# Kernel tuning notes

Measured on AMD Instinct MI355X. Metric: run time of the kernel, lower is better.

## Reference

```python
import jax, jax.numpy as jnp
import numpy as np

B, T, D, H, L, V = 2, 1024, 1024, 4, 4, 32000  # H redefined below
H = 16            # n_heads
HD = D // H       # head_size = 64
NL = 4            # n_layer
EPS = 1e-5


def _layernorm(x, scale, bias):
    mu = jnp.mean(x, axis=-1, keepdims=True)
    var = jnp.mean(jnp.square(x - mu), axis=-1, keepdims=True)
    return (x - mu) * jax.lax.rsqrt(var + EPS) * scale + bias


def setup_inputs() -> dict:
    key = jax.random.key(0)
    ks = iter(jax.random.split(key, 40))
    s = lambda shape: jax.random.normal(next(ks), shape, jnp.float32) * 0.02
    inp = {
        'idx': jax.random.randint(next(ks), (B, T), 0, V),
        'tok_emb': s((V, D)),
        'pos_emb': s((T, D)),
        # per-layer stacked params (leading axis = layer)
        'Wq': s((NL, D, D)), 'Wk': s((NL, D, D)), 'Wv': s((NL, D, D)),
        'Wo': s((NL, D, D)), 'bo': jnp.zeros((NL, D), jnp.float32),
        'ln1_s': jnp.ones((NL, D), jnp.float32), 'ln1_b': jnp.zeros((NL, D), jnp.float32),
        'ln2_s': jnp.ones((NL, D), jnp.float32), 'ln2_b': jnp.zeros((NL, D), jnp.float32),
        'W1': s((NL, D, 4 * D)), 'b1': jnp.zeros((NL, 4 * D), jnp.float32),
        'W2': s((NL, 4 * D, D)), 'b2': jnp.zeros((NL, D), jnp.float32),
        'lnf_s': jnp.ones((D,), jnp.float32), 'lnf_b': jnp.zeros((D,), jnp.float32),
        'Wlm': s((D, V)), 'blm': jnp.zeros((V,), jnp.float32),
    }
    return inp


def reference(idx, tok_emb, pos_emb, Wq, Wk, Wv, Wo, bo,
              ln1_s, ln1_b, ln2_s, ln2_b, W1, b1, W2, b2,
              lnf_s, lnf_b, Wlm, blm):
    b, t = idx.shape
    x = tok_emb[idx] + pos_emb[None, :t]            # [B,T,D]
    causal = jnp.tril(jnp.ones((t, t), bool))        # [T,T]
    scale = 1.0 / np.sqrt(HD).astype(np.float32)
    for l in range(NL):
        h = _layernorm(x, ln1_s[l], ln1_b[l])
        q = (h @ Wq[l]).reshape(b, t, H, HD)
        k = (h @ Wk[l]).reshape(b, t, H, HD)
        v = (h @ Wv[l]).reshape(b, t, H, HD)
        scores = jnp.einsum('bthd,bshd->bhts', q, k) * scale
        scores = jnp.where(causal[None, None], scores, -jnp.inf)
        attn = jax.nn.softmax(scores, axis=-1)       # [B,H,T,T]
        o = jnp.einsum('bhts,bshd->bthd', attn, v).reshape(b, t, D)
        x = x + o @ Wo[l] + bo[l]
        h2 = _layernorm(x, ln2_s[l], ln2_b[l])
        x = x + jax.nn.relu(h2 @ W1[l] + b1[l]) @ W2[l] + b2[l]
    x = _layernorm(x, lnf_s, lnf_b)
    logits = x @ Wlm + blm                           # [B,T,V]
    return logits
```

## Files before the change

### kernel.cpp

```cpp
#include <hip/hip_runtime.h>

typedef unsigned short u16;
typedef unsigned int u32;
typedef __bf16 bf16x8 __attribute__((ext_vector_type(8)));
typedef float f32x4 __attribute__((ext_vector_type(4)));
typedef u16 u16x8 __attribute__((ext_vector_type(8)));
typedef u16 u16x4 __attribute__((ext_vector_type(4)));

static __device__ __forceinline__ u16 f2bf(float f) {
  u32 u = __builtin_bit_cast(u32, f);
  u32 r = (u + 0x7FFFu + ((u >> 16) & 1u)) >> 16;
  return (u16)r;
}

static __device__ __forceinline__ void atomAddF32(float* p, float v) {
  asm volatile("global_atomic_add_f32 %0, %1, off" :: "v"(p), "v"(v) : "memory");
}

#define GLOAD_LDS16(gp, lp)                                                   \
  __builtin_amdgcn_global_load_lds(                                           \
      (const __attribute__((address_space(1))) void*)(gp),                    \
      (__attribute__((address_space(3))) void*)(lp), 16, 0, 0)

#define MFB(a, b, cc) __builtin_amdgcn_mfma_f32_16x16x32_bf16(a, b, cc, 0, 0, 0)

__global__ void k_embed_ln(const int* __restrict__ idx, const float* __restrict__ tok,
                           const float* __restrict__ pos, const float* __restrict__ sc,
                           const float* __restrict__ bi, float* __restrict__ x,
                           u16* __restrict__ out) {
  int row = blockIdx.x;
  int tt = row & 1023;
  int id = idx[row];
  int t = threadIdx.x;
  float4 a = *(const float4*)(tok + (size_t)id * 1024 + t * 4);
  float4 p = *(const float4*)(pos + (size_t)tt * 1024 + t * 4);
  float4 v{a.x + p.x, a.y + p.y, a.z + p.z, a.w + p.w};
  *(float4*)(x + (size_t)row * 1024 + t * 4) = v;
  float s = v.x + v.y + v.z + v.w;
  float ss = v.x * v.x + v.y * v.y + v.z * v.z + v.w * v.w;
  for (int d = 1; d < 64; d <<= 1) { s += __shfl_xor(s, d); ss += __shfl_xor(ss, d); }
  __shared__ float red[8];
  int wave = t >> 6, lane = t & 63;
  if (lane == 0) { red[wave] = s; red[wave + 4] = ss; }
  __syncthreads();
  s = red[0] + red[1] + red[2] + red[3];
  ss = red[4] + red[5] + red[6] + red[7];
  float mu = s * (1.0f / 1024.0f);
  float var = ss * (1.0f / 1024.0f) - mu * mu;
  float inv = rsqrtf(var + 1e-5f);
  float4 g = *(const float4*)(sc + t * 4);
  float4 b = *(const float4*)(bi + t * 4);
  u16x4 o;
  o[0] = f2bf((v.x - mu) * inv * g.x + b.x);
  o[1] = f2bf((v.y - mu) * inv * g.y + b.y);
  o[2] = f2bf((v.z - mu) * inv * g.z + b.z);
  o[3] = f2bf((v.w - mu) * inv * g.w + b.w);
  *(u16x4*)(out + (size_t)row * 1024 + t * 4) = o;
}

__global__ void k_ln(const float* __restrict__ x, const float* __restrict__ sc,
                     const float* __restrict__ bi, u16* __restrict__ out) {
  int row = blockIdx.x;
  int t = threadIdx.x;
  const float* xr = x + (size_t)row * 1024;
  float4 v = *(const float4*)(xr + t * 4);
  float s = v.x + v.y + v.z + v.w;
  float ss = v.x * v.x + v.y * v.y + v.z * v.z + v.w * v.w;
  for (int d = 1; d < 64; d <<= 1) { s += __shfl_xor(s, d); ss += __shfl_xor(ss, d); }
  __shared__ float red[8];
  int wave = t >> 6, lane = t & 63;
  if (lane == 0) { red[wave] = s; red[wave + 4] = ss; }
  __syncthreads();
  s = red[0] + red[1] + red[2] + red[3];
  ss = red[4] + red[5] + red[6] + red[7];
  float mu = s * (1.0f / 1024.0f);
  float var = ss * (1.0f / 1024.0f) - mu * mu;
  float inv = rsqrtf(var + 1e-5f);
  float4 g = *(const float4*)(sc + t * 4);
  float4 b = *(const float4*)(bi + t * 4);
  u16x4 o;
  o[0] = f2bf((v.x - mu) * inv * g.x + b.x);
  o[1] = f2bf((v.y - mu) * inv * g.y + b.y);
  o[2] = f2bf((v.z - mu) * inv * g.z + b.z);
  o[3] = f2bf((v.w - mu) * inv * g.w + b.w);
  *(u16x4*)(out + (size_t)row * 1024 + t * 4) = o;
}

__launch_bounds__(1024)
__global__ void k_transpose(const float* __restrict__ src, u16* __restrict__ dst,
                            int R, int C) {
  __shared__ float tile[32][33];
  int tx = threadIdx.x, ty = threadIdx.y;
  int c = blockIdx.x * 32 + tx;
  int r = blockIdx.y * 32 + ty;
  tile[ty][tx] = src[(size_t)r * C + c];
  __syncthreads();
  int dr = blockIdx.x * 32 + ty;
  int dc = blockIdx.y * 32 + tx;
  dst[(size_t)dr * R + dc] = f2bf(tile[tx][ty]);
}

__launch_bounds__(1024)
__global__ void k_transpose_layer(const float* __restrict__ Wq, const float* __restrict__ Wk,
                                  const float* __restrict__ Wv, const float* __restrict__ Wo,
                                  const float* __restrict__ W1, const float* __restrict__ W2,
                                  u16* __restrict__ qkvT, u16* __restrict__ WoT,
                                  u16* __restrict__ W1T, u16* __restrict__ W2T) {
  int bid = blockIdx.x;
  const float* src; u16* dst; int R, C, bx, by;
  if (bid < 4096) {
    int which = bid >> 10, tile_i = bid & 1023;
    bx = tile_i & 31; by = tile_i >> 5; R = 1024; C = 1024;
    src = which == 0 ? Wq : which == 1 ? Wk : which == 2 ? Wv : Wo;
    dst = which == 3 ? WoT : qkvT + (size_t)which * 1048576;
  } else if (bid < 8192) {
    int tile_i = bid - 4096; bx = tile_i & 127; by = tile_i >> 7; R = 1024; C = 4096;
    src = W1; dst = W1T;
  } else {
    int tile_i = bid - 8192; bx = tile_i & 31; by = tile_i >> 5; R = 4096; C = 1024;
    src = W2; dst = W2T;
  }
  __shared__ float tile[32][33];
  int tx = threadIdx.x, ty = threadIdx.y;
  int c = bx * 32 + tx, r = by * 32 + ty;
  tile[ty][tx] = src[(size_t)r * C + c];
  __syncthreads();
  int dr = bx * 32 + ty, dc = by * 32 + tx;
  dst[(size_t)dr * R + dc] = f2bf(tile[tx][ty]);
}

enum { EPI_QKV = 0, EPI_RELU = 2 };

template <int EPI>
__launch_bounds__(256, 4)
__global__ void k_gemm64(const u16* __restrict__ A, const u16* __restrict__ Bt,
                         const float* __restrict__ bias, u16* __restrict__ bout,
                         int M, int N, int K) {
  __shared__ alignas(16) u16 smem[12288];
#define AL(s, r, k) smem[(s)*2048 + (r)*32 + (k)]
#define BL(s, r, k) smem[4096 + (s)*4096 + (r)*32 + (k)]
  const int t = threadIdx.x;
  const int wave = t >> 6, lane = t & 63;
  const int wm = wave >> 1, wn = wave & 1;
  const int g = lane >> 4, c = lane & 15;
  const int m0 = blockIdx.x * 64, n0 = blockIdx.y * 128;

  const int rwA = t >> 2, sgA = (t & 3) * 8;
  const u16* gA = A + (size_t)(m0 + rwA) * K + sgA;
  const u16* gB = Bt + (size_t)(n0 + rwA) * K + sgA;

  f32x4 acc[2][4] = {};
  const int nK = K >> 5;
  int cur = 0;

  GLOAD_LDS16(gA, &AL(0, rwA, 0));
#pragma unroll
  for (int p = 0; p < 2; ++p)
    GLOAD_LDS16(gB + (size_t)p * 64 * K, &BL(0, p * 64 + rwA, 0));
  __syncthreads();

  for (int kt = 0; kt < nK; ++kt) {
    if (kt + 1 < nK) {
      const int k0 = (kt + 1) << 5;
      GLOAD_LDS16(gA + k0, &AL(cur ^ 1, rwA, 0));
#pragma unroll
      for (int p = 0; p < 2; ++p)
        GLOAD_LDS16(gB + k0 + (size_t)p * 64 * K, &BL(cur ^ 1, p * 64 + rwA, 0));
    }
    bf16x8 af[2], bfr[4];
#pragma unroll
    for (int i = 0; i < 2; ++i)
      af[i] = *(const bf16x8*)&AL(cur, wm * 32 + i * 16 + c, g * 8);
#pragma unroll
    for (int j = 0; j < 4; ++j)
      bfr[j] = *(const bf16x8*)&BL(cur, wn * 64 + j * 16 + c, g * 8);
#pragma unroll
    for (int i = 0; i < 2; ++i)
#pragma unroll
      for (int j = 0; j < 4; ++j)
        acc[i][j] = MFB(af[i], bfr[j], acc[i][j]);
    __syncthreads();
    cur ^= 1;
  }

  if (EPI == EPI_QKV) {
    const int which = n0 >> 10;
    const int b = m0 >> 10, t0 = m0 & 1023;
    const int hh0 = (n0 >> 6) & 15;
    if (which < 2) {
      const float qsc = (which == 0) ? 0.125f : 1.0f;
      u16 (*Ct)[136] = (u16(*)[136])smem;
#pragma unroll
      for (int i = 0; i < 2; ++i)
#pragma unroll
        for (int j = 0; j < 4; ++j)
#pragma unroll
          for (int r = 0; r < 4; ++r)
            Ct[wm * 32 + i * 16 + g * 4 + r][wn * 64 + j * 16 + c] = f2bf(acc[i][j][r] * qsc);
      __syncthreads();
      u16* obase = bout + (size_t)which * 2097152;
#pragma unroll
      for (int itr = 0; itr < 4; ++itr) {
        int idx2 = itr * 256 + t;
        int s = idx2 >> 9;
        int tt = (idx2 >> 3) & 63;
        int seg = idx2 & 7;
        u16x8 vv = *(const u16x8*)&Ct[tt][s * 64 + seg * 8];
        *(u16x8*)(obase + ((size_t)(b * 16 + hh0 + s) * 1024 + (t0 + tt)) * 64 + seg * 8) = vv;
      }
    } else {
      u16 (*Cv)[72] = (u16(*)[72])smem;
#pragma unroll
      for (int i = 0; i < 2; ++i)
#pragma unroll
        for (int j = 0; j < 4; ++j) {
          u16x4 pk;
#pragma unroll
          for (int r = 0; r < 4; ++r) pk[r] = f2bf(acc[i][j][r]);
          *(u16x4*)&Cv[wn * 64 + j * 16 + c][wm * 32 + i * 16 + g * 4] = pk;
        }
      __syncthreads();
      u16* obase = bout + (size_t)2 * 2097152;
#pragma unroll
      for (int itr = 0; itr < 4; ++itr) {
        int idx2 = itr * 256 + t;
        int row = idx2 >> 3;
        int seg = idx2 & 7;
        int s = row >> 6, f = row & 63;
        u16x8 vv = *(const u16x8*)&Cv[row][seg * 8];
        *(u16x8*)(obase + ((size_t)(b * 16 + hh0 + s) * 64 + f) * 1024 + t0 + seg * 8) = vv;
      }
    }
  } else {
    u16 (*Ct)[136] = (u16(*)[136])smem;
#pragma unroll
    for (int i = 0; i < 2; ++i)
#pragma unroll
      for (int j = 0; j < 4; ++j)
#pragma unroll
        for (int r = 0; r < 4; ++r) {
          float u = acc[i][j][r] + bias[n0 + wn * 64 + j * 16 + c];
          Ct[wm * 32 + i * 16 + g * 4 + r][wn * 64 + j * 16 + c] = f2bf(u > 0.f ? u : 0.f);
        }
    __syncthreads();
#pragma unroll
    for (int itr = 0; itr < 4; ++itr) {
      int idx2 = itr * 256 + t;
      int tt = idx2 >> 4, seg = idx2 & 15;
      *(u16x8*)(bout + (size_t)(m0 + tt) * N + n0 + seg * 8) =
          *(const u16x8*)&Ct[tt][seg * 8];
    }
  }
#undef AL
#undef BL
}

__launch_bounds__(256, 8)
__global__ void k_gemm_res(const u16* __restrict__ A, const u16* __restrict__ Bt,
                           const float* __restrict__ bias, float* __restrict__ fout,
                           int M, int N, int K) {
  __shared__ alignas(16) u16 smem[8192];
  const int t = threadIdx.x;
  const int wave = t >> 6, lane = t & 63;
  const int wm = wave >> 1, wn = wave & 1;
  const int g = lane >> 4, c = lane & 15;
  const int m0 = blockIdx.x * 64, n0 = blockIdx.y * 64;
  const int kz = blockIdx.z;
  const int Kh = K >> 1;
  const int kbase = kz * Kh;

  const int rw = t >> 2, sg = (t & 3) * 8;
  const u16* gA = A + (size_t)(m0 + rw) * K + kbase + sg;
  const u16* gB = Bt + (size_t)(n0 + rw) * K + kbase + sg;

  f32x4 acc[2][2] = {};
  const int nK = Kh >> 5;
  int cur = 0;

  GLOAD_LDS16(gA, &smem[rw * 32]);
  GLOAD_LDS16(gB, &smem[4096 + rw * 32]);
  __syncthreads();

  for (int kt = 0; kt < nK; ++kt) {
    if (kt + 1 < nK) {
      const int k0 = (kt + 1) << 5;
      GLOAD_LDS16(gA + k0, &smem[(cur ^ 1) * 2048 + rw * 32]);
      GLOAD_LDS16(gB + k0, &smem[4096 + (cur ^ 1) * 2048 + rw * 32]);
    }
    bf16x8 af[2], bfr[2];
#pragma unroll
    for (int i = 0; i < 2; ++i)
      af[i] = *(const bf16x8*)&smem[cur * 2048 + (wm * 32 + i * 16 + c) * 32 + g * 8];
#pragma unroll
    for (int j = 0; j < 2; ++j)
      bfr[j] = *(const bf16x8*)&smem[4096 + cur * 2048 + (wn * 32 + j * 16 + c) * 32 + g * 8];
#pragma unroll
    for (int i = 0; i < 2; ++i)
#pragma unroll
      for (int j = 0; j < 2; ++j)
        acc[i][j] = MFB(af[i], bfr[j], acc[i][j]);
    __syncthreads();
    cur ^= 1;
  }

#pragma unroll
  for (int i = 0; i < 2; ++i)
#pragma unroll
    for (int j = 0; j < 2; ++j)
#pragma unroll
      for (int r = 0; r < 4; ++r) {
        int m = m0 + wm * 32 + i * 16 + g * 4 + r;
        int n = n0 + wn * 32 + j * 16 + c;
        float v = acc[i][j][r] + (kz == 0 ? bias[n] : 0.f);
        atomAddF32(&fout[(size_t)m * N + n], v);
      }
}

__launch_bounds__(256, 4)
__global__ void k_gemm_out(const u16* __restrict__ A, const u16* __restrict__ Bt,
                           const float* __restrict__ bias, float* __restrict__ fout,
                           int M, int N, int K) {
  __shared__ alignas(16) u16 sm[2][2][128][32];
  const int t = threadIdx.x;
  const int wave = t >> 6, lane = t & 63;
  const int wm = wave >> 1, wn = wave & 1;
  const int g = lane >> 4, c = lane & 15;
  const int wg = (blockIdx.x & 7) * 500 + (blockIdx.x >> 3);
  const int m0 = (wg & 15) * 128, n0 = (wg >> 4) * 128;

  const int srow = wave * 32 + (lane >> 2);
  const int sseg = (lane & 3) * 8;
  const u16* gA = A + (size_t)(m0 + srow) * K + sseg;
  const u16* gB = Bt + (size_t)(n0 + srow) * K + sseg;

  f32x4 acc[4][4] = {};
  const int nK = K >> 5;
  int cur = 0;

#pragma unroll
  for (int p = 0; p < 2; ++p) {
    GLOAD_LDS16(gA + (size_t)p * 16 * K, &sm[0][0][wave * 32 + p * 16][0]);
    GLOAD_LDS16(gB + (size_t)p * 16 * K, &sm[0][1][wave * 32 + p * 16][0]);
  }
  __syncthreads();

  for (int kt = 0; kt < nK; ++kt) {
    if (kt + 1 < nK) {
      const int k0 = (kt + 1) << 5;
#pragma unroll
      for (int p = 0; p < 2; ++p) {
        GLOAD_LDS16(gA + k0 + (size_t)p * 16 * K, &sm[cur ^ 1][0][wave * 32 + p * 16][0]);
        GLOAD_LDS16(gB + k0 + (size_t)p * 16 * K, &sm[cur ^ 1][1][wave * 32 + p * 16][0]);
      }
    }
    bf16x8 af[4], bfr[4];
#pragma unroll
    for (int i = 0; i < 4; ++i) {
      af[i]  = *(const bf16x8*)&sm[cur][0][wm * 64 + i * 16 + c][g * 8];
      bfr[i] = *(const bf16x8*)&sm[cur][1][wn * 64 + i * 16 + c][g * 8];
    }
#pragma unroll
    for (int i = 0; i < 4; ++i)
#pragma unroll
      for (int j = 0; j < 4; ++j)
        acc[i][j] = MFB(af[i], bfr[j], acc[i][j]);
    __syncthreads();
    cur ^= 1;
  }

  float (*st)[132] = (float(*)[132])sm;
#pragma unroll
  for (int i = 0; i < 4; ++i) {
#pragma unroll
    for (int j = 0; j < 4; ++j)
#pragma unroll
      for (int r = 0; r < 4; ++r)
        st[wm * 16 + g * 4 + r][wn * 64 + j * 16 + c] = acc[i][j][r];
    __syncthreads();
    {
      int row = t >> 3;
      int cs = (t & 7) * 16;
      int m = m0 + (row >> 4) * 64 + i * 16 + (row & 15);
      float* dst = fout + (size_t)m * N + n0 + cs;
#pragma unroll
      for (int q = 0; q < 4; ++q) {
        float4 v = *(const float4*)&st[row][cs + q * 4];
        float4 bb = *(const float4*)&bias[n0 + cs + q * 4];
        float4 o{v.x + bb.x, v.y + bb.y, v.z + bb.z, v.w + bb.w};
        *(float4*)(dst + q * 4) = o;
      }
    }
    __syncthreads();
  }
}

#define AITER(ITV, MASKED)                                                    \
  {                                                                           \
    const int k0 = (ITV) << 5;                                                \
    bf16x8 kb0 = *(const bf16x8*)(Kh + (k0 + c) * 64 + g * 8);                \
    bf16x8 kb1 = *(const bf16x8*)(Kh + (k0 + c) * 64 + 32 + g * 8);           \
    bf16x8 kb2 = *(const bf16x8*)(Kh + (k0 + 16 + c) * 64 + g * 8);           \
    bf16x8 kb3 = *(const bf16x8*)(Kh + (k0 + 16 + c) * 64 + 32 + g * 8);      \
    bf16x8 bv0 = *(const bf16x8*)(VTh + (size_t)(c) * 1024 + k0 + g * 8);     \
    bf16x8 bv1 = *(const bf16x8*)(VTh + (size_t)(16 + c) * 1024 + k0 + g * 8);\
    bf16x8 bv2 = *(const bf16x8*)(VTh + (size_t)(32 + c) * 1024 + k0 + g * 8);\
    bf16x8 bv3 = *(const bf16x8*)(VTh + (size_t)(48 + c) * 1024 + k0 + g * 8);\
    f32x4 S[2][2];                                                            \
    __builtin_amdgcn_s_setprio(1);                                            \
    _Pragma("unroll") for (int qt = 0; qt < 2; ++qt) {                        \
      f32x4 z = {};                                                           \
      S[qt][0] = MFB(aq[qt][1], kb1, MFB(aq[qt][0], kb0, z));                 \
      S[qt][1] = MFB(aq[qt][1], kb3, MFB(aq[qt][0], kb2, z));                 \
    }                                                                         \
    __builtin_amdgcn_s_setprio(0);                                            \
    float sv[2][2][4], mt[2][4];                                              \
    float need = 0.0f;                                                        \
    _Pragma("unroll") for (int qt = 0; qt < 2; ++qt)                          \
      _Pragma("unroll") for (int r = 0; r < 4; ++r) {                         \
        float s0 = S[qt][0][r], s1 = S[qt][1][r];                             \
        if (MASKED) {                                                         \
          int q = q0 + qt * 16 + (g << 2) + r;                                \
          s0 = (k0 + c <= q) ? s0 : -1e30f;                                   \
          s1 = (k0 + 16 + c <= q) ? s1 : -1e30f;                              \
        }                                                                     \
        sv[qt][0][r] = s0; sv[qt][1][r] = s1;                                 \
        float m = fmaxf(s0, s1);                                              \
        m = fmaxf(m, __shfl_xor(m, 1));                                       \
        m = fmaxf(m, __shfl_xor(m, 2));                                       \
        m = fmaxf(m, __shfl_xor(m, 4));                                       \
        m = fmaxf(m, __shfl_xor(m, 8));                                       \
        mt[qt][r] = m;                                                        \
        need = fmaxf(need, m - Mr[qt][r]);                                    \
      }                                                                       \
    unsigned long long vote = __ballot(need <= 8.0f);                         \
    const bool nore = wv ? ((vote & 0xFFFFFFFF00000000ull) == 0xFFFFFFFF00000000ull) \
                         : ((vote & 0xFFFFFFFFull) == 0xFFFFFFFFull);         \
    _Pragma("unroll") for (int qt = 0; qt < 2; ++qt)                          \
      _Pragma("unroll") for (int r = 0; r < 4; ++r) {                         \
        float mn = nore ? Mr[qt][r] : fmaxf(Mr[qt][r], mt[qt][r]);            \
        float p0 = __expf(sv[qt][0][r] - mn);                                 \
        float p1 = __expf(sv[qt][1][r] - mn);                                 \
        if (nore) {                                                           \
          Lr[qt][r] += p0 + p1;         \
        } else {                                                              \
          float alpha = __expf(Mr[qt][r] - mn);                               \
          Lr[qt][r] = Lr[qt][r] * alpha + p0 + p1;                            \
          Mr[qt][r] = mn;                                                     \
          _Pragma("unroll") for (int nb = 0; nb < 4; ++nb) Oacc[qt][nb][r] *= alpha; \
        }                                                                     \
        Pl[wv][qt * 16 + (g << 2) + r][c] = f2bf(p0);                         \
        Pl[wv][qt * 16 + (g << 2) + r][16 + c] = f2bf(p1);                    \
      }                                                                       \
    __builtin_amdgcn_s_setprio(1);                                            \
    _Pragma("unroll") for (int qt = 0; qt < 2; ++qt) {                        \
      bf16x8 ap = *(const bf16x8*)&Pl[wv][qt * 16 + c][g * 8];                \
      Oacc[qt][0] = MFB(ap, bv0, Oacc[qt][0]);                                \
      Oacc[qt][1] = MFB(ap, bv1, Oacc[qt][1]);                                \
      Oacc[qt][2] = MFB(ap, bv2, Oacc[qt][2]);                                \
      Oacc[qt][3] = MFB(ap, bv3, Oacc[qt][3]);                                \
    }                                                                         \
    __builtin_amdgcn_s_setprio(0);                                            \
  }

__launch_bounds__(128)
__global__ void k_attn(const u16* __restrict__ Q, const u16* __restrict__ Kb,
                       const u16* __restrict__ VT, u16* __restrict__ O) {
  const int qb = blockIdx.x;
  const int bh = blockIdx.y;
  const int tid = threadIdx.x;
  const int wv = tid >> 6;
  const int lane = tid & 63;
  const int g = lane >> 4, c = lane & 15;
  const int q0 = qb << 5;
  const u16* Qh = Q + (size_t)bh * 65536;
  const u16* Kh = Kb + (size_t)bh * 65536;
  const u16* VTh = VT + (size_t)bh * 65536;

  __shared__ u16 Pl[2][32][40];
  __shared__ float mrg[64][48];

  bf16x8 aq[2][2];
#pragma unroll
  for (int qt = 0; qt < 2; ++qt) {
    aq[qt][0] = *(const bf16x8*)(Qh + (q0 + qt * 16 + c) * 64 + g * 8);
    aq[qt][1] = *(const bf16x8*)(Qh + (q0 + qt * 16 + c) * 64 + 32 + g * 8);
  }

  f32x4 Oacc[2][4] = {};
  float Mr[2][4], Lr[2][4] = {};
#pragma unroll
  for (int qt = 0; qt < 2; ++qt)
#pragma unroll
    for (int r = 0; r < 4; ++r) Mr[qt][r] = -1e30f;

  const int nIt = qb + 1;
  const int half = (nIt + 1) >> 1;

  if (wv == 0) {
    if (qb == 0) {
      AITER(0, 1);
    } else {
      for (int it = 0; it < half; ++it) AITER(it, 0);
    }
  } else {
    for (int it = half; it < nIt - 1; ++it) AITER(it, 0);
    if (qb >= 1) AITER(nIt - 1, 1);
  }

  if (wv == 1) {
#pragma unroll
    for (int qt = 0; qt < 2; ++qt) {
#pragma unroll
      for (int nb = 0; nb < 4; ++nb)
#pragma unroll
        for (int r = 0; r < 4; ++r)
          mrg[lane][qt * 16 + nb * 4 + r] = Oacc[qt][nb][r];
#pragma unroll
      for (int r = 0; r < 4; ++r) {
        mrg[lane][32 + qt * 4 + r] = Mr[qt][r];
        mrg[lane][40 + qt * 4 + r] = Lr[qt][r];
      }
    }
  }
  __syncthreads();
  if (wv == 0) {
    const int b = bh >> 4, hh = bh & 15;
#pragma unroll
    for (int qt = 0; qt < 2; ++qt)
#pragma unroll
      for (int r = 0; r < 4; ++r) {
        float m1 = mrg[lane][32 + qt * 4 + r];
        float l1 = mrg[lane][40 + qt * 4 + r];
        float mm = fmaxf(Mr[qt][r], m1);
        float a0 = __expf(Mr[qt][r] - mm);
        float a1 = __expf(m1 - mm);
        float l = a0 * Lr[qt][r] + a1 * l1;
        l += __shfl_xor(l, 1);
        l += __shfl_xor(l, 2);
        l += __shfl_xor(l, 4);
        l += __shfl_xor(l, 8);
        float invl = 1.0f / l;
        int tt = q0 + qt * 16 + (g << 2) + r;
#pragma unroll
        for (int nb = 0; nb < 4; ++nb) {
          float o1 = mrg[lane][qt * 16 + nb * 4 + r];
          float val = (a0 * Oacc[qt][nb][r] + a1 * o1) * invl;
          int d = nb * 16 + c;
          O[((size_t)(b * 1024 + tt)) * 1024 + hh * 64 + d] = f2bf(val);
        }
      }
  }
}

extern "C" void kernel_launch(void* const* d_in, const int* in_sizes, int n_in,
                              void* d_out, int out_size, void* d_ws, size_t ws_size,
                              hipStream_t stream) {
  const int*   idx  = (const int*)d_in[0];
  const float* tok  = (const float*)d_in[1];
  const float* pos  = (const float*)d_in[2];
  const float* Wq   = (const float*)d_in[3];
  const float* Wk   = (const float*)d_in[4];
  const float* Wv   = (const float*)d_in[5];
  const float* Wo   = (const float*)d_in[6];
  const float* bo   = (const float*)d_in[7];
  const float* ln1s = (const float*)d_in[8];
  const float* ln1b = (const float*)d_in[9];
  const float* ln2s = (const float*)d_in[10];
  const float* ln2b = (const float*)d_in[11];
  const float* W1   = (const float*)d_in[12];
  const float* b1   = (const float*)d_in[13];
  const float* W2   = (const float*)d_in[14];
  const float* b2   = (const float*)d_in[15];
  const float* lnfs = (const float*)d_in[16];
  const float* lnfb = (const float*)d_in[17];
  const float* Wlm  = (const float*)d_in[18];
  const float* blm  = (const float*)d_in[19];
  float* out = (float*)d_out;

  char* w = (char*)d_ws;
  auto alloc = [&](size_t bytes) {
    char* p = w;
    w += (bytes + 255) & ~(size_t)255;
    return p;
  };
  float* x  = (float*)alloc(2048ull * 1024 * 4);
  u16* h    = (u16*)alloc(2048ull * 1024 * 2);
  u16* qkv  = (u16*)alloc(3ull * 2097152 * 2);
  u16* o    = (u16*)alloc(2048ull * 1024 * 2);
  u16* a1   = (u16*)alloc(2048ull * 4096 * 2);
  u16* arena = (u16*)alloc(32000ull * 1024 * 2);

  dim3 b32(32, 32, 1);

  k_embed_ln<<<2048, 256, 0, stream>>>(idx, tok, pos, ln1s, ln1b, x, h);

  for (int l = 0; l < 4; ++l) {
    u16* qkvT = arena;
    u16* WoT  = arena + 3ull * 1048576;
    u16* W1T  = arena + 4ull * 1048576;
    u16* W2T  = arena + 8ull * 1048576;
    k_transpose_layer<<<12288, b32, 0, stream>>>(
        Wq + (size_t)l * 1048576, Wk + (size_t)l * 1048576,
        Wv + (size_t)l * 1048576, Wo + (size_t)l * 1048576,
        W1 + (size_t)l * 4194304, W2 + (size_t)l * 4194304,
        qkvT, WoT, W1T, W2T);

    if (l > 0)
      k_ln<<<2048, 256, 0, stream>>>(x, ln1s + l * 1024, ln1b + l * 1024, h);
    k_gemm64<EPI_QKV><<<dim3(32, 24), 256, 0, stream>>>(h, qkvT, nullptr, qkv,
                                                        2048, 3072, 1024);
    k_attn<<<dim3(32, 32), 128, 0, stream>>>(qkv, qkv + 2097152, qkv + 2 * 2097152, o);
    k_gemm_res<<<dim3(32, 16, 2), 256, 0, stream>>>(o, WoT, bo + l * 1024, x,
                                                    2048, 1024, 1024);
    k_ln<<<2048, 256, 0, stream>>>(x, ln2s + l * 1024, ln2b + l * 1024, h);
    k_gemm64<EPI_RELU><<<dim3(32, 32), 256, 0, stream>>>(h, W1T, b1 + l * 4096, a1,
                                                         2048, 4096, 1024);
    k_gemm_res<<<dim3(32, 16, 2), 256, 0, stream>>>(a1, W2T, b2 + l * 1024, x,
                                                    2048, 1024, 4096);
  }

  k_ln<<<2048, 256, 0, stream>>>(x, lnfs, lnfb, h);
  k_transpose<<<dim3(1000, 32), b32, 0, stream>>>(Wlm, arena, 1024, 32000);
  k_gemm_out<<<4000, 256, 0, stream>>>(h, arena, blm, out, 2048, 32000, 1024);
}
```

Before: 1.070 ms.

## Split attention KV range across four waves, reverse block order, deepen W2 split-K

```diff
diff --git a/kernel.cpp b/kernel.cpp
--- a/kernel.cpp
+++ b/kernel.cpp
@@ -266,7 +266,7 @@
   const int g = lane >> 4, c = lane & 15;
   const int m0 = blockIdx.x * 64, n0 = blockIdx.y * 64;
   const int kz = blockIdx.z;
-  const int Kh = K >> 1;
+  const int Kh = K / gridDim.z;
   const int kbase = kz * Kh;
 
   const int rw = t >> 2, sg = (t & 3) * 8;
@@ -432,9 +432,7 @@
         mt[qt][r] = m;                                                        \
         need = fmaxf(need, m - Mr[qt][r]);                                    \
       }                                                                       \
-    unsigned long long vote = __ballot(need <= 8.0f);                         \
-    const bool nore = wv ? ((vote & 0xFFFFFFFF00000000ull) == 0xFFFFFFFF00000000ull) \
-                         : ((vote & 0xFFFFFFFFull) == 0xFFFFFFFFull);         \
+    const bool nore = __all(need <= 8.0f);                                    \
     _Pragma("unroll") for (int qt = 0; qt < 2; ++qt)                          \
       _Pragma("unroll") for (int r = 0; r < 4; ++r) {                         \
         float mn = nore ? Mr[qt][r] : fmaxf(Mr[qt][r], mt[qt][r]);            \
@@ -462,10 +460,40 @@
     __builtin_amdgcn_s_setprio(0);                                            \
   }
 
-__launch_bounds__(128)
+#define PUBLISH(slot)                                                         \
+  {                                                                           \
+    _Pragma("unroll") for (int qt = 0; qt < 2; ++qt) {                        \
+      _Pragma("unroll") for (int nb = 0; nb < 4; ++nb)                        \
+        _Pragma("unroll") for (int r = 0; r < 4; ++r)                         \
+          pub[slot][lane][qt * 16 + nb * 4 + r] = Oacc[qt][nb][r];            \
+      _Pragma("unroll") for (int r = 0; r < 4; ++r) {                         \
+        pub[slot][lane][32 + qt * 4 + r] = Mr[qt][r];                         \
+        pub[slot][lane][40 + qt * 4 + r] = Lr[qt][r];                         \
+      }                                                                       \
+    }                                                                         \
+  }
+
+#define MERGEIN(slot)                                                         \
+  {                                                                           \
+    _Pragma("unroll") for (int qt = 0; qt < 2; ++qt)                          \
+      _Pragma("unroll") for (int r = 0; r < 4; ++r) {                         \
+        float m1 = pub[slot][lane][32 + qt * 4 + r];                          \
+        float l1 = pub[slot][lane][40 + qt * 4 + r];                          \
+        float mm = fmaxf(Mr[qt][r], m1);                                      \
+        float a0 = __expf(Mr[qt][r] - mm);                                    \
+        float a1 = __expf(m1 - mm);                                           \
+        Lr[qt][r] = a0 * Lr[qt][r] + a1 * l1;                                 \
+        Mr[qt][r] = mm;                                                       \
+        _Pragma("unroll") for (int nb = 0; nb < 4; ++nb)                      \
+          Oacc[qt][nb][r] = a0 * Oacc[qt][nb][r] +                            \
+                            a1 * pub[slot][lane][qt * 16 + nb * 4 + r];       \
+      }                                                                       \
+  }
+
+__launch_bounds__(256)
 __global__ void k_attn(const u16* __restrict__ Q, const u16* __restrict__ Kb,
                        const u16* __restrict__ VT, u16* __restrict__ O) {
-  const int qb = blockIdx.x;
+  const int qb = 31 - blockIdx.x;
   const int bh = blockIdx.y;
   const int tid = threadIdx.x;
   const int wv = tid >> 6;
@@ -476,8 +504,8 @@
   const u16* Kh = Kb + (size_t)bh * 65536;
   const u16* VTh = VT + (size_t)bh * 65536;
 
-  __shared__ u16 Pl[2][32][40];
-  __shared__ float mrg[64][48];
+  __shared__ u16 Pl[4][32][40];
+  __shared__ float pub[2][64][48];
 
   bf16x8 aq[2][2];
 #pragma unroll
@@ -494,47 +522,29 @@
     for (int r = 0; r < 4; ++r) Mr[qt][r] = -1e30f;
 
   const int nIt = qb + 1;
-  const int half = (nIt + 1) >> 1;
-
+  const int q4 = (nIt + 3) >> 2;
+  const int beg = wv * q4;
+  const int end = min(nIt, beg + q4);
+  const int endU = min(end, nIt - 1);
+  for (int it = beg; it < endU; ++it) AITER(it, 0);
+  if (beg < nIt && end == nIt) AITER(nIt - 1, 1);
+
+  if (wv == 1) PUBLISH(0);
+  if (wv == 3) PUBLISH(1);
+  __syncthreads();
+  if (wv == 0) MERGEIN(0);
+  if (wv == 2) MERGEIN(1);
+  __syncthreads();
+  if (wv == 2) PUBLISH(0);
+  __syncthreads();
   if (wv == 0) {
-    if (qb == 0) {
-      AITER(0, 1);
-    } else {
-      for (int it = 0; it < half; ++it) AITER(it, 0);
-    }
-  } else {
-    for (int it = half; it < nIt - 1; ++it) AITER(it, 0);
-    if (qb >= 1) AITER(nIt - 1, 1);
-  }
-
-  if (wv == 1) {
-#pragma unroll
-    for (int qt = 0; qt < 2; ++qt) {
-#pragma unroll
-      for (int nb = 0; nb < 4; ++nb)
-#pragma unroll
-        for (int r = 0; r < 4; ++r)
-          mrg[lane][qt * 16 + nb * 4 + r] = Oacc[qt][nb][r];
+    MERGEIN(0);
+    const int b = bh >> 4, hh = bh & 15;
+#pragma unroll
+    for (int qt = 0; qt < 2; ++qt)
 #pragma unroll
       for (int r = 0; r < 4; ++r) {
-        mrg[lane][32 + qt * 4 + r] = Mr[qt][r];
-        mrg[lane][40 + qt * 4 + r] = Lr[qt][r];
-      }
-    }
-  }
-  __syncthreads();
-  if (wv == 0) {
-    const int b = bh >> 4, hh = bh & 15;
-#pragma unroll
-    for (int qt = 0; qt < 2; ++qt)
-#pragma unroll
-      for (int r = 0; r < 4; ++r) {
-        float m1 = mrg[lane][32 + qt * 4 + r];
-        float l1 = mrg[lane][40 + qt * 4 + r];
-        float mm = fmaxf(Mr[qt][r], m1);
-        float a0 = __expf(Mr[qt][r] - mm);
-        float a1 = __expf(m1 - mm);
-        float l = a0 * Lr[qt][r] + a1 * l1;
+        float l = Lr[qt][r];
         l += __shfl_xor(l, 1);
         l += __shfl_xor(l, 2);
         l += __shfl_xor(l, 4);
@@ -543,10 +553,8 @@
         int tt = q0 + qt * 16 + (g << 2) + r;
 #pragma unroll
         for (int nb = 0; nb < 4; ++nb) {
-          float o1 = mrg[lane][qt * 16 + nb * 4 + r];
-          float val = (a0 * Oacc[qt][nb][r] + a1 * o1) * invl;
           int d = nb * 16 + c;
-          O[((size_t)(b * 1024 + tt)) * 1024 + hh * 64 + d] = f2bf(val);
+          O[((size_t)(b * 1024 + tt)) * 1024 + hh * 64 + d] = f2bf(Oacc[qt][nb][r] * invl);
         }
       }
   }
@@ -609,13 +617,13 @@
       k_ln<<<2048, 256, 0, stream>>>(x, ln1s + l * 1024, ln1b + l * 1024, h);
     k_gemm64<EPI_QKV><<<dim3(32, 24), 256, 0, stream>>>(h, qkvT, nullptr, qkv,
                                                         2048, 3072, 1024);
-    k_attn<<<dim3(32, 32), 128, 0, stream>>>(qkv, qkv + 2097152, qkv + 2 * 2097152, o);
+    k_attn<<<dim3(32, 32), 256, 0, stream>>>(qkv, qkv + 2097152, qkv + 2 * 2097152, o);
     k_gemm_res<<<dim3(32, 16, 2), 256, 0, stream>>>(o, WoT, bo + l * 1024, x,
                                                     2048, 1024, 1024);
     k_ln<<<2048, 256, 0, stream>>>(x, ln2s + l * 1024, ln2b + l * 1024, h);
     k_gemm64<EPI_RELU><<<dim3(32, 32), 256, 0, stream>>>(h, W1T, b1 + l * 4096, a1,
                                                          2048, 4096, 1024);
-    k_gemm_res<<<dim3(32, 16, 2), 256, 0, stream>>>(a1, W2T, b2 + l * 1024, x,
+    k_gemm_res<<<dim3(32, 16, 4), 256, 0, stream>>>(a1, W2T, b2 + l * 1024, x,
                                                     2048, 1024, 4096);
   }
 
```

New measurement: 1.135 ms. 1.06x slower.
